# Optimization experiments

Hardware: AMD Instinct MI355X
Metric: run time of the kernel (lower is better)

The kernel has to match this reference:

```python
import jax, jax.numpy as jnp
import numpy as np

B, T, H = 256, 2048, 128

def setup_inputs() -> dict:
    key = jax.random.key(0)
    ks = jax.random.split(key, 8)
    s = 1.0 / np.sqrt(H)  # PyTorch LSTM/Linear init: U(-1/sqrt(H), 1/sqrt(H))
    u = lambda k, shape: jax.random.uniform(k, shape, jnp.float32, -s, s)
    return {
        "x": jax.random.normal(ks[0], (B, T, 1), jnp.float32),
        "W_ih": u(ks[1], (4 * H, 1)),   # gate order: i, f, g, o
        "W_hh": u(ks[2], (4 * H, H)),
        "b_ih": u(ks[3], (4 * H,)),
        "b_hh": u(ks[4], (4 * H,)),
        "fc_w": u(ks[5], (1, H)),
        "fc_b": u(ks[6], (1,)),
    }

def _lstm(x, W_ih, W_hh, b_ih, b_hh):
    Bx = x.shape[0]
    Hh = W_hh.shape[1]
    # precompute input contribution to all gates: [B, T, 4H]
    xg = jnp.einsum('bti,gi->btg', x, W_ih) + b_ih + b_hh

    def step(carry, xg_t):
        h, c = carry
        g = xg_t + h @ W_hh.T                      # [B, 4H]
        i, f, gg, o = jnp.split(g, 4, axis=-1)
        i = jax.nn.sigmoid(i)
        f = jax.nn.sigmoid(f)
        gg = jnp.tanh(gg)
        o = jax.nn.sigmoid(o)
        c = f * c + i * gg
        h = o * jnp.tanh(c)
        return (h, c), h

    h0 = jnp.zeros((Bx, Hh), x.dtype)
    (hT, cT), hs = jax.lax.scan(step, (h0, h0), jnp.swapaxes(xg, 0, 1))
    return jnp.swapaxes(hs, 0, 1), hT, cT          # [B,T,H], [B,H], [B,H]

def reference(x, W_ih, W_hh, b_ih, b_hh, fc_w, fc_b):
    hs, hT, cT = _lstm(x, W_ih, W_hh, b_ih, b_hh)
    out = jnp.tanh(hs @ fc_w.T + fc_b)             # [B, T, 1]
    # num_layers=1 -> leading layer dim of 1 on h, c (PyTorch convention)
    return out, (hT[None], cT[None])
```

## Files before the change

### kernel.cpp

```cpp
#include <hip/hip_runtime.h>


typedef _Float16 half2v __attribute__((ext_vector_type(2)));
typedef _Float16 f16x8  __attribute__((ext_vector_type(8)));
typedef float    f32x4  __attribute__((ext_vector_type(4)));

constexpr int NB = 256;
constexpr int NT = 2048;
constexpr int NH = 128;

__device__ __forceinline__ float fexp2(float x) {
    float r;
    asm("v_exp_f32 %0, %1" : "=v"(r) : "v"(x));
    return r;
}
__device__ __forceinline__ float frcp(float x) {
    float r;
    asm("v_rcp_f32 %0, %1" : "=v"(r) : "v"(x));
    return r;
}
__device__ __forceinline__ float fsig(float x) {
    return frcp(1.f + fexp2(x * -1.44269504f));
}
__device__ __forceinline__ float ftanh(float x) {
    return fmaf(2.f, frcp(1.f + fexp2(x * -2.88539008f)), -1.f);
}

__device__ __forceinline__ unsigned packh2(float lo, float hi) {
    half2v p;
    p.x = (_Float16)lo;
    p.y = (_Float16)hi;
    return __builtin_bit_cast(unsigned, p);
}

__device__ __forceinline__ float dot2(unsigned int w, unsigned int h, float acc) {
    half2v a = __builtin_bit_cast(half2v, w);
    half2v b = __builtin_bit_cast(half2v, h);
#if __has_builtin(__builtin_amdgcn_fdot2)
    return __builtin_amdgcn_fdot2(a, b, acc, false);
#else
    float r;
    asm("v_dot2_f32_f16 %0, %1, %2, %3" : "=v"(r) : "v"(a), "v"(b), "v"(acc));
    return r;
#endif
}

__device__ __forceinline__ f32x4 mfma32(f16x8 a, f16x8 b, f32x4 c) {
#if __has_builtin(__builtin_amdgcn_mfma_f32_16x16x32_f16)
    return __builtin_amdgcn_mfma_f32_16x16x32_f16(a, b, c, 0, 0, 0);
#else
    asm("v_mfma_f32_16x16x32_f16 %0, %1, %2, %0" : "+v"(c) : "v"(a), "v"(b));
    return c;
#endif
}

__device__ __forceinline__ void barrier_lds() {
    asm volatile("s_waitcnt lgkmcnt(0)" ::: "memory");
    __builtin_amdgcn_s_barrier();
    asm volatile("" ::: "memory");
}

template <bool DEFER_FC>
__global__ __launch_bounds__(512, 2)
void lstm_k1(const float* __restrict__ x, const float* __restrict__ W_ih,
             const float* __restrict__ W_hh, const float* __restrict__ b_ih,
             const float* __restrict__ b_hh, const float* __restrict__ fc_w,
             const float* __restrict__ fc_b, float* __restrict__ out,
             _Float16* __restrict__ hws) {
    __shared__ __align__(16) float    x_lds[NT];
    __shared__ __align__(16) _Float16 h_lds[2][NH];
    __shared__ float red[8];

    const int b    = blockIdx.x;
    const int t    = threadIdx.x;
    const int lane = t & 63;
    const int w    = t >> 6;
    const int q    = lane >> 4;
    const int nlo  = lane & 15;
    const int u    = 16 * w + nlo;

    if (w < 4) __builtin_amdgcn_s_setprio(1);

    ((float4*)x_lds)[t] = ((const float4*)(x + (size_t)b * NT))[t];
    if (t < NH) h_lds[0][t] = (_Float16)0.f;

    f16x8 bw[4][4];
#pragma unroll
    for (int g = 0; g < 4; ++g) {
        const float* wrow = W_hh + (size_t)(g * NH + u) * NH;
#pragma unroll
        for (int kc = 0; kc < 4; ++kc) {
            float4 f0 = *(const float4*)(wrow + kc * 32 + q * 8);
            float4 f1 = *(const float4*)(wrow + kc * 32 + q * 8 + 4);
            f16x8 v;
            v[0] = (_Float16)f0.x; v[1] = (_Float16)f0.y;
            v[2] = (_Float16)f0.z; v[3] = (_Float16)f0.w;
            v[4] = (_Float16)f1.x; v[5] = (_Float16)f1.y;
            v[6] = (_Float16)f1.z; v[7] = (_Float16)f1.w;
            bw[g][kc] = v;
        }
    }
#pragma unroll
    for (int g = 0; g < 4; ++g)
#pragma unroll
        for (int kc = 0; kc < 4; ++kc) asm volatile("" : "+v"(bw[g][kc]));

    const float bi = b_ih[u] + b_hh[u];
    const float bf = b_ih[NH + u] + b_hh[NH + u];
    const float bz = b_ih[2 * NH + u] + b_hh[2 * NH + u];
    const float bo = b_ih[3 * NH + u] + b_hh[3 * NH + u];
    const float wi = W_ih[u];
    const float wf = W_ih[NH + u];
    const float wz = W_ih[2 * NH + u];
    const float wo = W_ih[3 * NH + u];

    float c = 0.f, h = 0.f;
    float fcw = 0.f, fcb = 0.f;
    if (!DEFER_FC) {
        fcw = fc_w[u];
        fcb = fc_b[0];
    }

    float*    outp = out + (size_t)b * NT;
    _Float16* hrow = DEFER_FC ? (hws + (size_t)b * NT * NH) : (_Float16*)nullptr;

    f32x4 ai = {0.f, 0.f, 0.f, 0.f}, af = ai, az = ai, ao = ai;

    __syncthreads();

    for (int step = 0; step < NT; ++step) {
        const _Float16* hbuf = h_lds[step & 1];
        float xv = x_lds[step];
        f16x8 av[4];
#pragma unroll
        for (int kc = 0; kc < 4; ++kc)
            av[kc] = *(const f16x8*)(hbuf + kc * 32 + q * 8);

        ai[0] = fmaf(xv, wi, bi);
        af[0] = fmaf(xv, wf, bf);
        az[0] = fmaf(xv, wz, bz);
        ao[0] = fmaf(xv, wo, bo);

#pragma unroll
        for (int kc = 0; kc < 4; ++kc) {
            ai = mfma32(av[kc], bw[0][kc], ai);
            af = mfma32(av[kc], bw[1][kc], af);
            az = mfma32(av[kc], bw[2][kc], az);
            ao = mfma32(av[kc], bw[3][kc], ao);
        }

        if (lane < 16) {
            float gi = fsig(ai[0]);
            float gf = fsig(af[0]);
            float gz = ftanh(az[0]);
            float go = fsig(ao[0]);
            c = fmaf(gf, c, gi * gz);
            h = go * ftanh(c);
            _Float16 hh = (_Float16)h;
            h_lds[(step + 1) & 1][u] = hh;
            if (DEFER_FC) hrow[(size_t)step * NH + u] = hh;
        }
        if (!DEFER_FC) {
            float p = (lane < 16) ? h * fcw : 0.f;
#pragma unroll
            for (int m = 8; m >= 1; m >>= 1) p += __shfl_xor(p, m, 64);
            if (lane == 0) red[w] = p;
            __syncthreads();
            if (t == 0) {
                float s = red[0] + red[1] + red[2] + red[3] + red[4] + red[5] +
                          red[6] + red[7];
                outp[step] = ftanh(s + fcb);
            }
        }
        barrier_lds();
    }

    if (lane < 16) {
        float* hT = out + (size_t)NB * NT;
        float* cT = hT + (size_t)NB * NH;
        hT[b * NH + u] = h;
        cT[b * NH + u] = c;
    }
}

__global__ __launch_bounds__(256) void fc_k2(const _Float16* __restrict__ hws,
                                             const float* __restrict__ fc_w,
                                             const float* __restrict__ fc_b,
                                             float* __restrict__ out) {
    __shared__ unsigned wlds[64];
    const int t = threadIdx.x;
    if (t < 64) {
        float2 f = ((const float2*)fc_w)[t];
        wlds[t] = packh2(f.x, f.y);
    }
    __syncthreads();

    const size_t idx = (size_t)blockIdx.x * 256 + t;
    const uint4* hp = (const uint4*)(hws + idx * NH);
    const uint4* wp = (const uint4*)wlds;
    float acc = 0.f;
#pragma unroll
    for (int j = 0; j < 16; ++j) {
        uint4 hv = hp[j];
        uint4 wv = wp[j];
        acc = dot2(hv.x, wv.x, acc);
        acc = dot2(hv.y, wv.y, acc);
        acc = dot2(hv.z, wv.z, acc);
        acc = dot2(hv.w, wv.w, acc);
    }
    out[idx] = ftanh(acc + fc_b[0]);
}

extern "C" void kernel_launch(void* const* d_in, const int* in_sizes, int n_in,
                              void* d_out, int out_size, void* d_ws, size_t ws_size,
                              hipStream_t stream) {
    const float* x    = (const float*)d_in[0];
    const float* W_ih = (const float*)d_in[1];
    const float* W_hh = (const float*)d_in[2];
    const float* b_ih = (const float*)d_in[3];
    const float* b_hh = (const float*)d_in[4];
    const float* fc_w = (const float*)d_in[5];
    const float* fc_b = (const float*)d_in[6];
    float* out = (float*)d_out;

    const size_t need = (size_t)NB * NT * NH * sizeof(_Float16);
    if (ws_size >= need) {
        _Float16* hws = (_Float16*)d_ws;
        lstm_k1<true><<<dim3(NB), dim3(512), 0, stream>>>(
            x, W_ih, W_hh, b_ih, b_hh, fc_w, fc_b, out, hws);
        fc_k2<<<dim3(NB * NT / 256), dim3(256), 0, stream>>>(hws, fc_w, fc_b, out);
    } else {
        lstm_k1<false><<<dim3(NB), dim3(512), 0, stream>>>(
            x, W_ih, W_hh, b_ih, b_hh, fc_w, fc_b, out, nullptr);
    }
}
```

Measured before the change: 902.1 us.

## Split LSTM gate activations across half-waves and stop resetting MFMA accumulators

Gate activations are now divided between two 16-lane groups. Lanes in the lower half compute the i and f gates and lanes in the upper half compute g and o. The results are exchanged with permlane32_swap, so the serial activation chain on each lane is shorter. The accumulators are also no longer reinitialised with the input projection before the MFMAs. Each step instead takes the difference from the previous accumulated value and adds the input term afterwards, which removes a write-before-MFMA dependency. The cost is extra cross-lane traffic and some fp32 precision loss, because the accumulators grow over 2048 steps.

```diff
diff --git a/kernel.cpp b/kernel.cpp
--- a/kernel.cpp
+++ b/kernel.cpp
@@ -18,9 +18,6 @@
     float r;
     asm("v_rcp_f32 %0, %1" : "=v"(r) : "v"(x));
     return r;
-}
-__device__ __forceinline__ float fsig(float x) {
-    return frcp(1.f + fexp2(x * -1.44269504f));
 }
 __device__ __forceinline__ float ftanh(float x) {
     return fmaf(2.f, frcp(1.f + fexp2(x * -2.88539008f)), -1.f);
@@ -51,6 +48,19 @@
 #else
     asm("v_mfma_f32_16x16x32_f16 %0, %1, %2, %0" : "+v"(c) : "v"(a), "v"(b));
     return c;
+#endif
+}
+
+__device__ __forceinline__ float xswap32(float x, bool pick0) {
+#if __has_builtin(__builtin_amdgcn_permlane32_swap)
+    unsigned xu = __builtin_bit_cast(unsigned, x);
+    auto rr = __builtin_amdgcn_permlane32_swap(xu, xu, false, false);
+    unsigned t2[2];
+    __builtin_memcpy(t2, &rr, 8);
+    return __builtin_bit_cast(float, pick0 ? t2[0] : t2[1]);
+#else
+    (void)pick0;
+    return __shfl_xor(x, 32, 64);
 #endif
 }
 
@@ -78,8 +88,20 @@
     const int q    = lane >> 4;
     const int nlo  = lane & 15;
     const int u    = 16 * w + nlo;
+    const int half = (lane >> 5) & 1;
 
     if (w < 4) __builtin_amdgcn_s_setprio(1);
+
+    bool pick0 = false;
+#if __has_builtin(__builtin_amdgcn_permlane32_swap)
+    {
+        unsigned lid = (unsigned)lane;
+        auto pr = __builtin_amdgcn_permlane32_swap(lid, lid, false, false);
+        unsigned p2[2];
+        __builtin_memcpy(p2, &pr, 8);
+        pick0 = (p2[0] != lid);
+    }
+#endif
 
     ((float4*)x_lds)[t] = ((const float4*)(x + (size_t)b * NT))[t];
     if (t < NH) h_lds[0][t] = (_Float16)0.f;
@@ -105,16 +127,16 @@
 #pragma unroll
         for (int kc = 0; kc < 4; ++kc) asm volatile("" : "+v"(bw[g][kc]));
 
-    const float bi = b_ih[u] + b_hh[u];
-    const float bf = b_ih[NH + u] + b_hh[NH + u];
-    const float bz = b_ih[2 * NH + u] + b_hh[2 * NH + u];
-    const float bo = b_ih[3 * NH + u] + b_hh[3 * NH + u];
-    const float wi = W_ih[u];
-    const float wf = W_ih[NH + u];
-    const float wz = W_ih[2 * NH + u];
-    const float wo = W_ih[3 * NH + u];
+    const int g0row = (half ? 2 : 0) * NH + u;
+    const int g1row = (half ? 3 : 1) * NH + u;
+    const float bias0 = b_ih[g0row] + b_hh[g0row];
+    const float bias1 = b_ih[g1row] + b_hh[g1row];
+    const float wih0  = W_ih[g0row];
+    const float wih1  = W_ih[g1row];
+    const float kmul0 = half ? -2.88539008f : -1.44269504f;
 
     float c = 0.f, h = 0.f;
+    float prev0 = 0.f, prev1 = 0.f;
     float fcw = 0.f, fcb = 0.f;
     if (!DEFER_FC) {
         fcw = fc_w[u];
@@ -135,11 +157,6 @@
 #pragma unroll
         for (int kc = 0; kc < 4; ++kc)
             av[kc] = *(const f16x8*)(hbuf + kc * 32 + q * 8);
-
-        ai[0] = fmaf(xv, wi, bi);
-        af[0] = fmaf(xv, wf, bf);
-        az[0] = fmaf(xv, wz, bz);
-        ao[0] = fmaf(xv, wo, bo);
 
 #pragma unroll
         for (int kc = 0; kc < 4; ++kc) {
@@ -149,13 +166,24 @@
             ao = mfma32(av[kc], bw[3][kc], ao);
         }
 
+        float s_i = ai[0], s_f = af[0], s_z = az[0], s_o = ao[0];
+        float d0 = half ? s_z : s_i;
+        float d1 = half ? s_o : s_f;
+        float pre0 = fmaf(xv, wih0, (d0 - prev0) + bias0);
+        float pre1 = fmaf(xv, wih1, (d1 - prev1) + bias1);
+        prev0 = d0;
+        prev1 = d1;
+        float r0   = frcp(1.f + fexp2(pre0 * kmul0));
+        float act0 = half ? fmaf(2.f, r0, -1.f) : r0;
+        float act1 = frcp(1.f + fexp2(pre1 * -1.44269504f));
+        float oth0 = xswap32(act0, pick0);
+        float oth1 = xswap32(act1, pick0);
+        float gf = half ? oth1 : act1;
+        float go = half ? act1 : oth1;
+        c = fmaf(gf, c, act0 * oth0);
+        h = go * ftanh(c);
+
         if (lane < 16) {
-            float gi = fsig(ai[0]);
-            float gf = fsig(af[0]);
-            float gz = ftanh(az[0]);
-            float go = fsig(ao[0]);
-            c = fmaf(gf, c, gi * gz);
-            h = go * ftanh(c);
             _Float16 hh = (_Float16)h;
             h_lds[(step + 1) & 1][u] = hh;
             if (DEFER_FC) hrow[(size_t)step * NH + u] = hh;
```

Result: slower. 970.4 us (+7.6%).
